# Optimization experiments

Hardware: AMD Instinct MI355X
Metric: run time of the kernel (lower is better)

## Reference

```python
import jax, jax.numpy as jnp
import numpy as np

TEMPERATURE = 0.07
EPS = 1e-12  # F.normalize eps
DIAG_FILL = -10.0


def _l1_normalize(x):
    # F.normalize(x, p=1, dim=-1): x / max(sum|x|, eps)
    denom = jnp.maximum(jnp.sum(jnp.abs(x), axis=-1, keepdims=True), EPS)
    return x / denom


def setup_inputs() -> dict:
    key = jax.random.key(0)
    k1, k2 = jax.random.split(key)
    B, D, H, W = 4, 128, 64, 64
    feat_q = jax.random.normal(k1, (B, D, H, W), dtype=jnp.float32)
    feat_k = jax.random.normal(k2, (B, D, H, W), dtype=jnp.float32)
    return {"feat_q": feat_q, "feat_k": feat_k}


def reference(feat_q, feat_k):
    B, D = feat_q.shape[0], feat_q.shape[1]
    # [B, D, H, W] -> [B, N, D]
    q = feat_q.reshape(B, D, -1).transpose(0, 2, 1)
    k = feat_k.reshape(B, D, -1).transpose(0, 2, 1)
    q = _l1_normalize(q)
    k = _l1_normalize(k)
    k = jax.lax.stop_gradient(k)  # feat_k.detach()
    N = q.shape[1]
    # similarity matrix [B, N, N]
    sim = jnp.einsum('bnd,bmd->bnm', q, k)
    eye = jnp.eye(N, dtype=bool)
    sim = jnp.where(eye[None, :, :], DIAG_FILL, sim)
    logits = sim.reshape(-1, N) / TEMPERATURE  # negatives
    # out = concat([zeros, logits]); CE with target 0 => loss row = logsumexp(out) - 0
    lse = jax.nn.logsumexp(logits, axis=-1)
    loss = jnp.mean(jnp.logaddexp(jnp.float32(0.0), lse))
    return loss
```

## Files before the change

kernel.cpp:

```cpp
#include <hip/hip_runtime.h>

#define NB 4
#define DD 128
#define NN 4096
#define INV_T 14.285714285714285f

typedef __attribute__((ext_vector_type(8))) short bf16x8;
typedef __attribute__((ext_vector_type(4))) float f32x4;

static __device__ __forceinline__ unsigned short f32_to_bf16(float x){
  unsigned u = __float_as_uint(x);
  u += 0x7fffu + ((u >> 16) & 1u);
  return (unsigned short)(u >> 16);
}

static __device__ __forceinline__ void async_copy16(const uint4* g, uint4* l){
  __builtin_amdgcn_global_load_lds(
      (const __attribute__((address_space(1))) unsigned int*)g,
      (__attribute__((address_space(3))) unsigned int*)l, 16, 0, 0);
}

__global__ __launch_bounds__(256) void norm_kernel(const float* __restrict__ fq,
                                                   const float* __restrict__ fk,
                                                   unsigned short* __restrict__ qn,
                                                   unsigned short* __restrict__ kn){
  const float* src = blockIdx.z ? fk : fq;
  unsigned short* dst = blockIdx.z ? kn : qn;
  int b = blockIdx.y;
  int n0 = blockIdx.x * 64;
  __shared__ float sT[64][129];
  __shared__ float red[4][64];
  __shared__ float srd[64];
  int t = threadIdx.x;
  const float* sb = src + (size_t)b*DD*NN + n0;
  #pragma unroll
  for (int it = 0; it < 32; ++it){
    int idx = it*256 + t;
    int d = idx >> 6, nn = idx & 63;
    sT[nn][d] = sb[(size_t)d*NN + nn];
  }
  __syncthreads();
  {
    int nn = t & 63, part = t >> 6;
    float s = 0.f;
    #pragma unroll
    for (int j = 0; j < 32; ++j) s += fabsf(sT[nn][part*32 + j]);
    red[part][nn] = s;
  }
  __syncthreads();
  if (t < 64){
    float dsum = red[0][t] + red[1][t] + red[2][t] + red[3][t];
    srd[t] = 1.f / fmaxf(dsum, 1e-12f);
  }
  __syncthreads();
  unsigned short* db = dst + ((size_t)b*NN + n0)*DD;
  #pragma unroll
  for (int it = 0; it < 4; ++it){
    int c = it*256 + t;
    int row = c >> 4, dc = c & 15;
    float r = srd[row];
    unsigned v[4];
    #pragma unroll
    for (int p = 0; p < 4; ++p){
      unsigned short lo = f32_to_bf16(sT[row][dc*8 + p*2    ] * r);
      unsigned short hi = f32_to_bf16(sT[row][dc*8 + p*2 + 1] * r);
      v[p] = (unsigned)lo | ((unsigned)hi << 16);
    }
    uint4 pack = make_uint4(v[0], v[1], v[2], v[3]);
    int sw = dc ^ (row & 15);
    *reinterpret_cast<uint4*>(db + (size_t)row*DD + sw*8) = pack;
  }
}

__global__ __launch_bounds__(256,2) void simexp_kernel(const unsigned short* __restrict__ qn,
                                                       const unsigned short* __restrict__ kn,
                                                       float* __restrict__ rowsum){
  __shared__ uint4 sQ[2048];
  __shared__ uint4 sK[2048];
  int t = threadIdx.x;
  int w = t >> 6, lane = t & 63;
  int quad = lane >> 4, l16 = lane & 15;
  int b  = blockIdx.z;
  int r0 = blockIdx.x * 128;
  int c0 = blockIdx.y * 1024;
  const uint4* gq = reinterpret_cast<const uint4*>(qn + ((size_t)b*NN + r0)*DD);
  const uint4* gk = reinterpret_cast<const uint4*>(kn + ((size_t)b*NN + c0)*DD);
  #pragma unroll
  for (int i = 0; i < 8; ++i)
    async_copy16(gq + w*512 + i*64 + lane, &sQ[w*512 + i*64]);
  #pragma unroll
  for (int i = 0; i < 8; ++i)
    async_copy16(gk + w*512 + i*64 + lane, &sK[w*512 + i*64]);
  __syncthreads();

  int wr = (w >> 1)*64, wc = (w & 1)*64;
  bf16x8 a[4][4];
  #pragma unroll
  for (int i = 0; i < 4; ++i){
    int row = wr + i*16 + l16;
    #pragma unroll
    for (int ks = 0; ks < 4; ++ks)
      a[i][ks] = __builtin_bit_cast(bf16x8, sQ[row*16 + ((ks*4 + quad) ^ l16)]);
  }
  float rsum[16];
  #pragma unroll
  for (int s = 0; s < 16; ++s) rsum[s] = 0.f;

  for (int kt = 0; kt < 8; ++kt){
    if (kt){
      __syncthreads();
      #pragma unroll
      for (int i = 0; i < 8; ++i)
        async_copy16(gk + kt*2048 + w*512 + i*64 + lane, &sK[w*512 + i*64]);
      __syncthreads();
    }
    f32x4 acc[4][4];
    #pragma unroll
    for (int i = 0; i < 4; ++i)
      #pragma unroll
      for (int j = 0; j < 4; ++j)
        acc[i][j] = (f32x4){0.f, 0.f, 0.f, 0.f};
    #pragma unroll
    for (int ks = 0; ks < 4; ++ks){
      bf16x8 bfr[4];
      #pragma unroll
      for (int j = 0; j < 4; ++j){
        int col = wc + j*16 + l16;
        bfr[j] = __builtin_bit_cast(bf16x8, sK[col*16 + ((ks*4 + quad) ^ l16)]);
      }
      #pragma unroll
      for (int i = 0; i < 4; ++i)
        #pragma unroll
        for (int j = 0; j < 4; ++j)
          acc[i][j] = __builtin_amdgcn_mfma_f32_16x16x32_bf16(a[i][ks], bfr[j], acc[i][j], 0, 0, 0);
    }
    #pragma unroll
    for (int i = 0; i < 4; ++i)
      #pragma unroll
      for (int j = 0; j < 4; ++j)
        #pragma unroll
        for (int r = 0; r < 4; ++r)
          rsum[i*4 + r] += __expf(acc[i][j][r] * INV_T);
  }
  #pragma unroll
  for (int s = 0; s < 16; ++s){
    float v = rsum[s];
    v += __shfl_xor(v, 1, 64);
    v += __shfl_xor(v, 2, 64);
    v += __shfl_xor(v, 4, 64);
    v += __shfl_xor(v, 8, 64);
    if (l16 == 0){
      int row = r0 + wr + (s >> 2)*16 + quad*4 + (s & 3);
      atomicAdd(&rowsum[b*NN + row], v);
    }
  }
}

__global__ __launch_bounds__(256) void finalize_kernel(const unsigned short* __restrict__ qn,
                                                       const unsigned short* __restrict__ kn,
                                                       const float* __restrict__ rowsum,
                                                       float* __restrict__ out){
  int idx = blockIdx.x*256 + threadIdx.x;
  const uint4* q = reinterpret_cast<const uint4*>(qn + (size_t)idx*DD);
  const uint4* k = reinterpret_cast<const uint4*>(kn + (size_t)idx*DD);
  float dot = 0.f;
  #pragma unroll
  for (int c = 0; c < 16; ++c){
    uint4 uq = q[c], uk = k[c];
    unsigned aq[4] = {uq.x, uq.y, uq.z, uq.w};
    unsigned ak[4] = {uk.x, uk.y, uk.z, uk.w};
    #pragma unroll
    for (int p = 0; p < 4; ++p){
      float q0 = __uint_as_float(aq[p] << 16);
      float q1 = __uint_as_float(aq[p] & 0xffff0000u);
      float k0 = __uint_as_float(ak[p] << 16);
      float k1 = __uint_as_float(ak[p] & 0xffff0000u);
      dot = fmaf(q0, k0, dot);
      dot = fmaf(q1, k1, dot);
    }
  }
  float diag = __expf(dot * INV_T);
  float loss = log1pf(rowsum[idx] - diag);
  loss += __shfl_xor(loss, 1, 64);
  loss += __shfl_xor(loss, 2, 64);
  loss += __shfl_xor(loss, 4, 64);
  loss += __shfl_xor(loss, 8, 64);
  loss += __shfl_xor(loss, 16, 64);
  loss += __shfl_xor(loss, 32, 64);
  if ((threadIdx.x & 63) == 0)
    atomicAdd(out, loss * (1.f / (float)(NB*NN)));
}

extern "C" void kernel_launch(void* const* d_in, const int* in_sizes, int n_in,
                              void* d_out, int out_size, void* d_ws, size_t ws_size,
                              hipStream_t stream){
  const float* fq = (const float*)d_in[0];
  const float* fk = (const float*)d_in[1];
  unsigned short* qn = (unsigned short*)d_ws;
  unsigned short* kn = qn + (size_t)NB*NN*DD;
  float* rowsum = (float*)(kn + (size_t)NB*NN*DD);
  float* out = (float*)d_out;

  hipMemsetAsync(rowsum, 0, (size_t)NB*NN*sizeof(float), stream);
  hipMemsetAsync(out, 0, sizeof(float), stream);

  norm_kernel<<<dim3(NN/64, NB, 2), 256, 0, stream>>>(fq, fk, qn, kn);
  simexp_kernel<<<dim3(NN/128, 4, NB), 256, 0, stream>>>(qn, kn, rowsum);
  finalize_kernel<<<dim3(NB*NN/256), 256, 0, stream>>>(qn, kn, rowsum, out);
}
```

Baseline: 100.4 us.

## Double-buffer K tiles, mask diagonal in-tile, fold memsets into norm kernel

The K tile loads in the similarity kernel are now double-buffered, so the next tile is fetched asynchronously while the current one is computed, with one barrier per iteration instead of two. The diagonal is masked directly inside the MFMA accumulators, which lets the finalize kernel drop its separate per-row q·k recomputation. The two memsets are folded into the normalization kernel, which also switches to float4 global loads, and exp is computed via exp2f with a prescaled constant. The risks are the correctness of the zeroing order across kernels and of the diagonal lane mapping.

```diff
diff --git a/kernel.cpp b/kernel.cpp
--- a/kernel.cpp
+++ b/kernel.cpp
@@ -4,6 +4,7 @@
 #define DD 128
 #define NN 4096
 #define INV_T 14.285714285714285f
+#define EXP2C 20.60992915555662f
 
 typedef __attribute__((ext_vector_type(8))) short bf16x8;
 typedef __attribute__((ext_vector_type(4))) float f32x4;
@@ -23,21 +24,29 @@
 __global__ __launch_bounds__(256) void norm_kernel(const float* __restrict__ fq,
                                                    const float* __restrict__ fk,
                                                    unsigned short* __restrict__ qn,
-                                                   unsigned short* __restrict__ kn){
+                                                   unsigned short* __restrict__ kn,
+                                                   float* __restrict__ rowsum,
+                                                   float* __restrict__ out){
   const float* src = blockIdx.z ? fk : fq;
   unsigned short* dst = blockIdx.z ? kn : qn;
   int b = blockIdx.y;
   int n0 = blockIdx.x * 64;
+  int t = threadIdx.x;
+  if (blockIdx.z == 0 && t < 64) rowsum[b*NN + n0 + t] = 0.f;
+  if (blockIdx.z == 0 && blockIdx.x == 0 && b == 0 && t == 64) *out = 0.f;
   __shared__ float sT[64][129];
   __shared__ float red[4][64];
   __shared__ float srd[64];
-  int t = threadIdx.x;
   const float* sb = src + (size_t)b*DD*NN + n0;
   #pragma unroll
-  for (int it = 0; it < 32; ++it){
+  for (int it = 0; it < 8; ++it){
     int idx = it*256 + t;
-    int d = idx >> 6, nn = idx & 63;
-    sT[nn][d] = sb[(size_t)d*NN + nn];
+    int d = idx >> 4, g = idx & 15;
+    const float4 v = *reinterpret_cast<const float4*>(sb + (size_t)d*NN + g*4);
+    sT[g*4+0][d] = v.x;
+    sT[g*4+1][d] = v.y;
+    sT[g*4+2][d] = v.z;
+    sT[g*4+3][d] = v.w;
   }
   __syncthreads();
   {
@@ -75,8 +84,8 @@
 __global__ __launch_bounds__(256,2) void simexp_kernel(const unsigned short* __restrict__ qn,
                                                        const unsigned short* __restrict__ kn,
                                                        float* __restrict__ rowsum){
-  __shared__ uint4 sQ[2048];
-  __shared__ uint4 sK[2048];
+  __shared__ uint4 sA[2048];
+  __shared__ uint4 sB[2048];
   int t = threadIdx.x;
   int w = t >> 6, lane = t & 63;
   int quad = lane >> 4, l16 = lane & 15;
@@ -87,10 +96,10 @@
   const uint4* gk = reinterpret_cast<const uint4*>(kn + ((size_t)b*NN + c0)*DD);
   #pragma unroll
   for (int i = 0; i < 8; ++i)
-    async_copy16(gq + w*512 + i*64 + lane, &sQ[w*512 + i*64]);
+    async_copy16(gq + w*512 + i*64 + lane, &sA[w*512 + i*64]);
   #pragma unroll
   for (int i = 0; i < 8; ++i)
-    async_copy16(gk + w*512 + i*64 + lane, &sK[w*512 + i*64]);
+    async_copy16(gk + w*512 + i*64 + lane, &sB[w*512 + i*64]);
   __syncthreads();
 
   int wr = (w >> 1)*64, wc = (w & 1)*64;
@@ -100,19 +109,21 @@
     int row = wr + i*16 + l16;
     #pragma unroll
     for (int ks = 0; ks < 4; ++ks)
-      a[i][ks] = __builtin_bit_cast(bf16x8, sQ[row*16 + ((ks*4 + quad) ^ l16)]);
-  }
+      a[i][ks] = __builtin_bit_cast(bf16x8, sA[row*16 + ((ks*4 + quad) ^ l16)]);
+  }
+  __syncthreads();
+
   float rsum[16];
   #pragma unroll
   for (int s = 0; s < 16; ++s) rsum[s] = 0.f;
 
   for (int kt = 0; kt < 8; ++kt){
-    if (kt){
-      __syncthreads();
+    const uint4* rd  = (kt & 1) ? sA : sB;
+    uint4*       wrb = (kt & 1) ? sB : sA;
+    if (kt < 7){
       #pragma unroll
       for (int i = 0; i < 8; ++i)
-        async_copy16(gk + kt*2048 + w*512 + i*64 + lane, &sK[w*512 + i*64]);
-      __syncthreads();
+        async_copy16(gk + (kt+1)*2048 + w*512 + i*64 + lane, &wrb[w*512 + i*64]);
     }
     f32x4 acc[4][4];
     #pragma unroll
@@ -126,7 +137,7 @@
       #pragma unroll
       for (int j = 0; j < 4; ++j){
         int col = wc + j*16 + l16;
-        bfr[j] = __builtin_bit_cast(bf16x8, sK[col*16 + ((ks*4 + quad) ^ l16)]);
+        bfr[j] = __builtin_bit_cast(bf16x8, rd[col*16 + ((ks*4 + quad) ^ l16)]);
       }
       #pragma unroll
       for (int i = 0; i < 4; ++i)
@@ -134,13 +145,23 @@
         for (int j = 0; j < 4; ++j)
           acc[i][j] = __builtin_amdgcn_mfma_f32_16x16x32_bf16(a[i][ks], bfr[j], acc[i][j], 0, 0, 0);
     }
+    if ((c0 + kt*128 == r0) && (wr == wc)){
+      bool hit = (quad == (l16 >> 2));
+      int rr = l16 & 3;
+      #pragma unroll
+      for (int i = 0; i < 4; ++i)
+        #pragma unroll
+        for (int r = 0; r < 4; ++r)
+          acc[i][i][r] = (hit && r == rr) ? -1e38f : acc[i][i][r];
+    }
     #pragma unroll
     for (int i = 0; i < 4; ++i)
       #pragma unroll
       for (int j = 0; j < 4; ++j)
         #pragma unroll
         for (int r = 0; r < 4; ++r)
-          rsum[i*4 + r] += __expf(acc[i][j][r] * INV_T);
+          rsum[i*4 + r] += exp2f(acc[i][j][r] * EXP2C);
+    __syncthreads();
   }
   #pragma unroll
   for (int s = 0; s < 16; ++s){
@@ -156,31 +177,10 @@
   }
 }
 
-__global__ __launch_bounds__(256) void finalize_kernel(const unsigned short* __restrict__ qn,
-                                                       const unsigned short* __restrict__ kn,
-                                                       const float* __restrict__ rowsum,
+__global__ __launch_bounds__(256) void finalize_kernel(const float* __restrict__ rowsum,
                                                        float* __restrict__ out){
   int idx = blockIdx.x*256 + threadIdx.x;
-  const uint4* q = reinterpret_cast<const uint4*>(qn + (size_t)idx*DD);
-  const uint4* k = reinterpret_cast<const uint4*>(kn + (size_t)idx*DD);
-  float dot = 0.f;
-  #pragma unroll
-  for (int c = 0; c < 16; ++c){
-    uint4 uq = q[c], uk = k[c];
-    unsigned aq[4] = {uq.x, uq.y, uq.z, uq.w};
-    unsigned ak[4] = {uk.x, uk.y, uk.z, uk.w};
-    #pragma unroll
-    for (int p = 0; p < 4; ++p){
-      float q0 = __uint_as_float(aq[p] << 16);
-      float q1 = __uint_as_float(aq[p] & 0xffff0000u);
-      float k0 = __uint_as_float(ak[p] << 16);
-      float k1 = __uint_as_float(ak[p] & 0xffff0000u);
-      dot = fmaf(q0, k0, dot);
-      dot = fmaf(q1, k1, dot);
-    }
-  }
-  float diag = __expf(dot * INV_T);
-  float loss = log1pf(rowsum[idx] - diag);
+  float loss = log1pf(rowsum[idx]);
   loss += __shfl_xor(loss, 1, 64);
   loss += __shfl_xor(loss, 2, 64);
   loss += __shfl_xor(loss, 4, 64);
@@ -201,10 +201,7 @@
   float* rowsum = (float*)(kn + (size_t)NB*NN*DD);
   float* out = (float*)d_out;
 
-  hipMemsetAsync(rowsum, 0, (size_t)NB*NN*sizeof(float), stream);
-  hipMemsetAsync(out, 0, sizeof(float), stream);
-
-  norm_kernel<<<dim3(NN/64, NB, 2), 256, 0, stream>>>(fq, fk, qn, kn);
+  norm_kernel<<<dim3(NN/64, NB, 2), 256, 0, stream>>>(fq, fk, qn, kn, rowsum, out);
   simexp_kernel<<<dim3(NN/128, 4, NB), 256, 0, stream>>>(qn, kn, rowsum);
-  finalize_kernel<<<dim3(NB*NN/256), 256, 0, stream>>>(qn, kn, rowsum, out);
-}
+  finalize_kernel<<<dim3(NB*NN/256), 256, 0, stream>>>(rowsum, out);
+}
```

New measurement: 99.06 us, median of 2. About the same (-1.3%).
